# Kernel tuning notes

Hardware: AMD Instinct MI355X
Metric: run time of the kernel (lower is better)

## Reference

```python
import jax, jax.numpy as jnp
import numpy as np

B, T, D, H = 2, 2048, 1024, 16
HD = D // H            # 64
FH = 2752              # SwiGLU hidden: round64(int(2*4*D/3))
BETA_INIT = 0.5


def rmsnorm(x, w, eps=1e-6):
    x32 = x.astype(jnp.float32)
    r = jax.lax.rsqrt(jnp.mean(x32 * x32, axis=-1, keepdims=True) + eps)
    return (x32 * r).astype(x.dtype) * w


def rope(x, cos, sin):
    # x: (B,H,T,HD); cos/sin: (T,HD//2)
    d2 = x.shape[-1] // 2
    x1, x2 = x[..., :d2], x[..., d2:]
    return jnp.concatenate([x1 * cos - x2 * sin, x2 * cos + x1 * sin], axis=-1)


def delta_res(x, h, gn_w, g_w, g_b, wv_w, eps_k=1e-6):
    # k-hat = normalize(h); k = k_hat / sqrt(d)
    h32 = h.astype(jnp.float32)
    nrm = jnp.sqrt(jnp.sum(h32 * h32, axis=-1, keepdims=True))
    k = (h32 / jnp.maximum(nrm, eps_k)).astype(x.dtype) * (1.0 / np.sqrt(D))
    c = rmsnorm(x, gn_w)
    logit = c @ g_w + g_b                                   # (B,T)
    beta = (2.0 * jax.nn.sigmoid(logit.astype(jnp.float32))).astype(x.dtype)[..., None]
    v = jax.nn.sigmoid(x @ wv_w)[..., None]                 # (B,T,1)
    kTx = jnp.sum(k * x, axis=-1, keepdims=True)
    return x + beta * (v - kTx) * k


def setup_inputs() -> dict:
    key = jax.random.key(0)
    ks = jax.random.split(key, 12)
    s = 0.02
    gb = np.float32(np.log(BETA_INIT / 2.0 / (1.0 - BETA_INIT / 2.0 + 1e-8)))
    return {
        "x": jax.random.normal(ks[0], (B, T, D), jnp.float32),
        "wq": jax.random.normal(ks[1], (D, D), jnp.float32) * s,
        "wk": jax.random.normal(ks[2], (D, D), jnp.float32) * s,
        "wv": jax.random.normal(ks[3], (D, D), jnp.float32) * s,
        "wo": jax.random.normal(ks[4], (D, D), jnp.float32) * s,
        "qn_w": jnp.ones((HD,), jnp.float32),
        "kn_w": jnp.ones((HD,), jnp.float32),
        "attn_norm_w": jnp.ones((D,), jnp.float32),
        "g1_norm_w": jnp.ones((D,), jnp.float32),
        "g1_w": jax.random.normal(ks[5], (D,), jnp.float32) * s,
        "g1_b": jnp.asarray(gb),
        "wv1": jax.random.normal(ks[6], (D,), jnp.float32) * s,
        "mlp_norm_w": jnp.ones((D,), jnp.float32),
        "w1": jax.random.normal(ks[7], (FH, D), jnp.float32) * s,
        "w2": jax.random.normal(ks[8], (D, FH), jnp.float32) * s,
        "w3": jax.random.normal(ks[9], (FH, D), jnp.float32) * s,
        "g2_norm_w": jnp.ones((D,), jnp.float32),
        "g2_w": jax.random.normal(ks[10], (D,), jnp.float32) * s,
        "g2_b": jnp.asarray(gb),
        "wv2": jax.random.normal(ks[11], (D,), jnp.float32) * s,
    }


def reference(x, wq, wk, wv, wo, qn_w, kn_w, attn_norm_w,
              g1_norm_w, g1_w, g1_b, wv1, mlp_norm_w, w1, w2, w3,
              g2_norm_w, g2_w, g2_b, wv2):
    # ---- attention sublayer (pre-norm) ----
    xc = rmsnorm(x, attn_norm_w)
    q = (xc @ wq.T).reshape(B, T, H, HD).swapaxes(1, 2)   # (B,H,T,HD)
    k = (xc @ wk.T).reshape(B, T, H, HD).swapaxes(1, 2)
    v = (xc @ wv.T).reshape(B, T, H, HD).swapaxes(1, 2)
    q = rmsnorm(q, qn_w)
    k = rmsnorm(k, kn_w)
    inv_freq = 1.0 / (10000.0 ** (jnp.arange(0, HD, 2, dtype=jnp.float32) / HD))
    freqs = jnp.arange(T, dtype=jnp.float32)[:, None] * inv_freq[None, :]  # (T,HD/2)
    cos, sin = jnp.cos(freqs), jnp.sin(freqs)
    q = rope(q, cos, sin)
    k = rope(k, cos, sin)
    scale = 1.0 / np.sqrt(HD)
    scores = jnp.einsum('bhqd,bhkd->bhqk', q, k) * scale
    causal = jnp.where(jnp.arange(T)[:, None] >= jnp.arange(T)[None, :], 0.0, -jnp.inf).astype(scores.dtype)
    attn = jax.nn.softmax(scores + causal, axis=-1)
    out = jnp.einsum('bhqk,bhkd->bhqd', attn, v)
    h_attn = out.swapaxes(1, 2).reshape(B, T, D) @ wo.T
    x = delta_res(x, h_attn, g1_norm_w, g1_w, g1_b, wv1)
    # ---- MLP sublayer (pre-norm SwiGLU) ----
    xm = rmsnorm(x, mlp_norm_w)
    h_mlp = (jax.nn.silu(xm @ w1.T) * (xm @ w3.T)) @ w2.T
    x = delta_res(x, h_mlp, g2_norm_w, g2_w, g2_b, wv2)
    return x
```

## Files before the change

kernel.cpp:

```cpp
#include <hip/hip_runtime.h>
#include <hip/hip_bf16.h>
#include <math.h>

using bf16 = __hip_bfloat16;
typedef __bf16 bf16x8 __attribute__((ext_vector_type(8)));
typedef float f32x4 __attribute__((ext_vector_type(4)));

static constexpr int B_ = 2, T_ = 2048, D_ = 1024, H_ = 16, HD_ = 64, FH_ = 2752;
static constexpr int BT = B_ * T_;

struct __align__(8)  bh4 { bf16 h[4]; };
struct __align__(16) bh8 { bf16 h[8]; };

#define DEV static __device__ __forceinline__

DEV float b2f(bf16 v) { return __bfloat162float(v); }
DEV bf16  f2b(float v) { return __float2bfloat16(v); }
DEV __bf16 f2bb(float f) { __hip_bfloat16 h = __float2bfloat16(f); return *reinterpret_cast<__bf16*>(&h); }
DEV float sigmoidf_(float x) { return 1.0f / (1.0f + __expf(-x)); }

DEV void load4f(const bf16* p, float* v) {
    bh4 t = *reinterpret_cast<const bh4*>(p);
#pragma unroll
    for (int i = 0; i < 4; ++i) v[i] = b2f(t.h[i]);
}
DEV void load4f(const float* p, float* v) {
    float4 t = *reinterpret_cast<const float4*>(p);
    v[0] = t.x; v[1] = t.y; v[2] = t.z; v[3] = t.w;
}
DEV void store4(float* p, const float* v) {
    float4 t; t.x = v[0]; t.y = v[1]; t.z = v[2]; t.w = v[3];
    *reinterpret_cast<float4*>(p) = t;
}
DEV float waveReduceSum(float v) {
#pragma unroll
    for (int m = 32; m; m >>= 1) v += __shfl_xor(v, m);
    return v;
}

DEV void gl_lds16(const bf16* g, bf16* lds_base) {
    __builtin_amdgcn_global_load_lds(
        (const __attribute__((address_space(1))) void*)g,
        (__attribute__((address_space(3))) void*)lds_base, 16, 0, 0);
}

__global__ __launch_bounds__(256) void k_rope_tables(float* __restrict__ cost, float* __restrict__ sint) {
    int idx = blockIdx.x * 256 + threadIdx.x;
    if (idx >= T_ * 32) return;
    int t = idx >> 5, j = idx & 31;
    float inv = powf(10000.0f, -(float)j * (1.0f / 32.0f));
    float f = (float)t * inv;
    cost[idx] = cosf(f);
    sint[idx] = sinf(f);
}

__global__ __launch_bounds__(256) void k_f2b(const float* __restrict__ in, bf16* __restrict__ out, int n8) {
    int i = blockIdx.x * 256 + threadIdx.x;
    if (i >= n8) return;
    const float4* p = reinterpret_cast<const float4*>(in + (size_t)i * 8);
    float4 a = p[0], b = p[1];
    bh8 o;
    o.h[0] = f2b(a.x); o.h[1] = f2b(a.y); o.h[2] = f2b(a.z); o.h[3] = f2b(a.w);
    o.h[4] = f2b(b.x); o.h[5] = f2b(b.y); o.h[6] = f2b(b.z); o.h[7] = f2b(b.w);
    *reinterpret_cast<bh8*>(out + (size_t)i * 8) = o;
}

__global__ __launch_bounds__(256) void k_f2b_pair(const float* __restrict__ w1, const float* __restrict__ w3,
                                                  bf16* __restrict__ outp, int n8tot) {
    int i = blockIdx.x * 256 + threadIdx.x;
    if (i >= n8tot) return;
    int r = i >> 7, c8 = i & 127;
    int sel = (r >> 4) & 1;
    int j = ((r >> 5) << 4) | (r & 15);
    const float* src = (sel ? w3 : w1) + (size_t)j * D_ + c8 * 8;
    float4 a = reinterpret_cast<const float4*>(src)[0];
    float4 b = reinterpret_cast<const float4*>(src)[1];
    bh8 o;
    o.h[0] = f2b(a.x); o.h[1] = f2b(a.y); o.h[2] = f2b(a.z); o.h[3] = f2b(a.w);
    o.h[4] = f2b(b.x); o.h[5] = f2b(b.y); o.h[6] = f2b(b.z); o.h[7] = f2b(b.w);
    *reinterpret_cast<bh8*>(outp + (size_t)r * D_ + c8 * 8) = o;
}

__global__ __launch_bounds__(256) void k_rmsnorm(const float* __restrict__ x, const float* __restrict__ w,
                                                 bf16* __restrict__ out) {
    int row = blockIdx.x, tid = threadIdx.x;
    const float* xr = x + (size_t)row * D_;
    int base = tid * 4;
    float v[4];
    load4f(xr + base, v);
    float ss = v[0]*v[0] + v[1]*v[1] + v[2]*v[2] + v[3]*v[3];
    ss = waveReduceSum(ss);
    __shared__ float red[4];
    if ((tid & 63) == 0) red[tid >> 6] = ss;
    __syncthreads();
    ss = red[0] + red[1] + red[2] + red[3];
    float r = rsqrtf(ss * (1.0f / D_) + 1e-6f);
    float wv[4];
    load4f(w + base, wv);
    bh4 o;
#pragma unroll
    for (int i = 0; i < 4; ++i) o.h[i] = f2b(v[i] * r * wv[i]);
    *reinterpret_cast<bh4*>(out + (size_t)row * D_ + base) = o;
}

template <int BN, int EPI>
__global__ __launch_bounds__(256) void k_gemm_db(const bf16* __restrict__ A, const bf16* __restrict__ W,
                                                 bf16* __restrict__ C, int M, int N, int K) {
    constexpr int MR = (BN == 128) ? 4 : 2;
    constexpr int WR = (BN == 128) ? 64 : 32;
    __shared__ bf16 sA[2][128 * 32];
    __shared__ bf16 sB[2][BN * 32];
    int tid = threadIdx.x, lane = tid & 63, wid = tid >> 6;
    int m0 = blockIdx.x * 128, n0 = blockIdx.y * BN;
    int wr, wc;
    if (BN == 128) { wr = wid >> 1; wc = wid & 1; } else { wr = wid; wc = 0; }
    int l16 = lane & 15, lg = lane >> 4;
    int srow = lane >> 2;
    int scol = ((lane & 3) ^ (srow & 3)) * 8;
    int rchunk = (lg ^ (l16 & 3)) * 8;

    f32x4 acc[MR][4] = {};

#define STAGE(buf, k0)                                                                  \
    {                                                                                   \
        _Pragma("unroll")                                                               \
        for (int c = 0; c < 2; ++c) {                                                   \
            int r0 = wid * 32 + c * 16;                                                 \
            gl_lds16(&A[(size_t)(m0 + r0 + srow) * K + (k0) + scol], &sA[buf][r0 * 32]);\
        }                                                                               \
        if (BN == 128) {                                                                \
            _Pragma("unroll")                                                           \
            for (int c = 0; c < 2; ++c) {                                               \
                int r0 = wid * 32 + c * 16;                                             \
                int nrow = n0 + r0 + srow;                                              \
                if (nrow > N - 1) nrow = N - 1;                                         \
                gl_lds16(&W[(size_t)nrow * K + (k0) + scol], &sB[buf][r0 * 32]);        \
            }                                                                           \
        } else {                                                                        \
            int r0 = wid * 16;                                                          \
            int nrow = n0 + r0 + srow;                                                  \
            if (nrow > N - 1) nrow = N - 1;                                             \
            gl_lds16(&W[(size_t)nrow * K + (k0) + scol], &sB[buf][r0 * 32]);            \
        }                                                                               \
    }

    STAGE(0, 0);
    __syncthreads();
    int nk = K >> 5;
    int cur = 0;
    for (int t = 0; t < nk; ++t) {
        if (t + 1 < nk) STAGE(cur ^ 1, (t + 1) * 32);
        bf16x8 af[MR], bfr[4];
#pragma unroll
        for (int m = 0; m < MR; ++m)
            af[m] = *reinterpret_cast<const bf16x8*>(&sA[cur][(wr * WR + m * 16 + l16) * 32 + rchunk]);
#pragma unroll
        for (int n = 0; n < 4; ++n)
            bfr[n] = *reinterpret_cast<const bf16x8*>(&sB[cur][(wc * 64 + n * 16 + l16) * 32 + rchunk]);
#pragma unroll
        for (int m = 0; m < MR; ++m)
#pragma unroll
            for (int n = 0; n < 4; ++n)
                acc[m][n] = __builtin_amdgcn_mfma_f32_16x16x32_bf16(af[m], bfr[n], acc[m][n], 0, 0, 0);
        __syncthreads();
        cur ^= 1;
    }
#undef STAGE

    int rbase = m0 + wr * WR, cbase = n0 + wc * 64;
    if (EPI == 1) {
        int Ng = N >> 1;
        int gbase = (n0 >> 1) + wc * 32;
#pragma unroll
        for (int m = 0; m < MR; ++m) {
#pragma unroll
            for (int n2 = 0; n2 < 2; ++n2) {
                int gcol = gbase + n2 * 16 + l16;
#pragma unroll
                for (int r = 0; r < 4; ++r) {
                    int row = rbase + m * 16 + lg * 4 + r;
                    float a1 = acc[m][n2 * 2][r];
                    float a3 = acc[m][n2 * 2 + 1][r];
                    C[(size_t)row * Ng + gcol] = f2b(a1 * sigmoidf_(a1) * a3);
                }
            }
        }
    } else {
#pragma unroll
        for (int m = 0; m < MR; ++m) {
#pragma unroll
            for (int n = 0; n < 4; ++n) {
                int col = cbase + n * 16 + l16;
                if (col < N) {
#pragma unroll
                    for (int r = 0; r < 4; ++r) {
                        int row = rbase + m * 16 + lg * 4 + r;
                        C[(size_t)row * N + col] = f2b(acc[m][n][r]);
                    }
                }
            }
        }
    }
}

__global__ __launch_bounds__(256) void k_qk_norm_rope(const bf16* __restrict__ qin, const float* __restrict__ wn,
                                                      const float* __restrict__ cost, const float* __restrict__ sint,
                                                      bf16* __restrict__ qout, float scale, int ld, int off) {
    int tid = threadIdx.x;
    int g = blockIdx.x * 4 + (tid >> 6);
    int d = tid & 63;
    int h = g % H_, t = (g / H_) % T_, b = g / (H_ * T_);
    float v = b2f(qin[(size_t)(b * T_ + t) * ld + off + h * HD_ + d]);
    float ss = waveReduceSum(v * v);
    float r = rsqrtf(ss * (1.0f / HD_) + 1e-6f);
    float xn = v * r * wn[d];
    float p = __shfl_xor(xn, 32);
    float c = cost[t * 32 + (d & 31)], s = sint[t * 32 + (d & 31)];
    float o = (d < 32) ? (xn * c - p * s) : (xn * c + p * s);
    qout[((size_t)(b * H_ + h) * T_ + t) * HD_ + d] = f2b(o * scale);
}

__global__ __launch_bounds__(256) void k_v_transpose(const bf16* __restrict__ vin, bf16* __restrict__ vt,
                                                     int ld, int off) {
    __shared__ bf16 tile[64][72];
    int tid = threadIdx.x;
    int bh = blockIdx.y;
    int t0 = blockIdx.x * 64;
    int b = bh >> 4, h = bh & 15;
#pragma unroll
    for (int i = 0; i < 16; ++i) {
        int lin = i * 256 + tid;
        int tl = lin >> 6, d = lin & 63;
        tile[tl][d] = vin[(size_t)(b * T_ + t0 + tl) * ld + off + h * HD_ + d];
    }
    __syncthreads();
#pragma unroll
    for (int i = 0; i < 16; ++i) {
        int lin = i * 256 + tid;
        int d = lin >> 6, tl = lin & 63;
        vt[((size_t)bh * HD_ + d) * T_ + t0 + tl] = tile[tl][d];
    }
}

template <bool MASKED>
DEV void fa3_tile(const bf16* __restrict__ kl, const bf16* __restrict__ vl,
                  int l16, int lg, int qloc,
                  const bf16x8 qf0, const bf16x8 qf1,
                  f32x4* acc, float& m_r, float& l_r) {
    f32x4 s[8];
#pragma unroll
    for (int n = 0; n < 8; ++n) {
        int kv = n * 16 + l16;
        bf16x8 kf0 = *reinterpret_cast<const bf16x8*>(&kl[kv * 64 + (((lg ^ kv) & 7) << 3)]);
        bf16x8 kf1 = *reinterpret_cast<const bf16x8*>(&kl[kv * 64 + ((((4 + lg) ^ kv) & 7) << 3)]);
        f32x4 t = {};
        t = __builtin_amdgcn_mfma_f32_16x16x32_bf16(kf0, qf0, t, 0, 0, 0);
        t = __builtin_amdgcn_mfma_f32_16x16x32_bf16(kf1, qf1, t, 0, 0, 0);
        s[n] = t;
    }
    if (MASKED) {
#pragma unroll
        for (int n = 0; n < 8; ++n)
#pragma unroll
            for (int r = 0; r < 4; ++r)
                if (n * 16 + lg * 4 + r > qloc) s[n][r] = -INFINITY;
    }
    float mx = -INFINITY;
#pragma unroll
    for (int n = 0; n < 8; ++n)
#pragma unroll
        for (int r = 0; r < 4; ++r) mx = fmaxf(mx, s[n][r]);
    mx = fmaxf(mx, __shfl_xor(mx, 16));
    mx = fmaxf(mx, __shfl_xor(mx, 32));
    float mnew = fmaxf(m_r, mx);
    float corr = __expf(m_r - mnew);
    m_r = mnew;
    float ps = 0.0f;
#pragma unroll
    for (int n = 0; n < 8; ++n)
#pragma unroll
        for (int r = 0; r < 4; ++r) {
            float e = __expf(s[n][r] - mnew);
            s[n][r] = e;
            ps += e;
        }
    l_r = l_r * corr + ps;
#pragma unroll
    for (int np = 0; np < 4; ++np) acc[np] = acc[np] * corr;

    bf16x8 pb[4];
#pragma unroll
    for (int n2 = 0; n2 < 4; ++n2)
#pragma unroll
        for (int j = 0; j < 8; ++j)
            pb[n2][j] = f2bb(s[2 * n2 + (j >> 2)][j & 3]);

    int d15 = l16;
    int eoff = (lg & 1) * 4;
#pragma unroll
    for (int n2 = 0; n2 < 4; ++n2) {
        int c0 = (n2 * 4 + (lg >> 1));
        int c1 = c0 + 2;
#pragma unroll
        for (int np = 0; np < 4; ++np) {
            int d = np * 16 + l16;
            union { bf16x8 v; bh4 q[2]; } u;
            u.q[0] = *reinterpret_cast<const bh4*>(&vl[d * 128 + ((c0 ^ d15) << 3) + eoff]);
            u.q[1] = *reinterpret_cast<const bh4*>(&vl[d * 128 + ((c1 ^ d15) << 3) + eoff]);
            acc[np] = __builtin_amdgcn_mfma_f32_16x16x32_bf16(u.v, pb[n2], acc[np], 0, 0, 0);
        }
    }
}

__global__ __launch_bounds__(256) void k_flash(const bf16* __restrict__ Q, const bf16* __restrict__ Kk,
                                               const bf16* __restrict__ Vt, bf16* __restrict__ Out) {
    __shared__ bf16 kl[128 * 64];
    __shared__ bf16 vl[64 * 128];
    int tid = threadIdx.x, lane = tid & 63, w = tid >> 6;
    int l16 = lane & 15, lg = lane >> 4;
    int L = blockIdx.x;
    int xcd = L & 7, m = L >> 3;
    int bh = xcd * 4 + (m & 3);
    int qi = (T_ / 128 - 1) - (m >> 2);
    int q0 = qi * 128;
    int b = bh >> 4, h = bh & 15;
    const bf16* qb = Q + (size_t)bh * T_ * HD_;
    const bf16* kb = Kk + (size_t)bh * T_ * HD_;
    const bf16* vb = Vt + (size_t)bh * HD_ * T_;

    bf16x8 qfr[2][2];
#pragma unroll
    for (int f = 0; f < 2; ++f) {
        int qrow = q0 + w * 32 + f * 16 + l16;
        const bf16* qp = qb + (size_t)qrow * HD_ + lg * 8;
        qfr[f][0] = *reinterpret_cast<const bf16x8*>(qp);
        qfr[f][1] = *reinterpret_cast<const bf16x8*>(qp + 32);
    }
    f32x4 acc[2][4] = {};
    float m_r[2] = {-INFINITY, -INFINITY};
    float l_r[2] = {0.0f, 0.0f};

    for (int kv0 = 0; kv0 <= q0; kv0 += 128) {
        __syncthreads();
#pragma unroll
        for (int i = 0; i < 4; ++i) {
            int idx = i * 256 + tid;
            int kv = idx >> 3, c = idx & 7;
            *reinterpret_cast<bh8*>(&kl[kv * 64 + (((c ^ kv) & 7) << 3)]) =
                *reinterpret_cast<const bh8*>(&kb[(size_t)(kv0 + kv) * HD_ + c * 8]);
        }
#pragma unroll
        for (int i = 0; i < 4; ++i) {
            int idx = i * 256 + tid;
            int d = idx >> 4, c = idx & 15;
            *reinterpret_cast<bh8*>(&vl[d * 128 + (((c ^ d) & 15) << 3)]) =
                *reinterpret_cast<const bh8*>(&vb[(size_t)d * T_ + kv0 + c * 8]);
        }
        __syncthreads();
        if (kv0 == q0) {
#pragma unroll
            for (int f = 0; f < 2; ++f)
                fa3_tile<true>(kl, vl, l16, lg, w * 32 + f * 16 + l16,
                               qfr[f][0], qfr[f][1], acc[f], m_r[f], l_r[f]);
        } else {
#pragma unroll
            for (int f = 0; f < 2; ++f)
                fa3_tile<false>(kl, vl, l16, lg, 0,
                                qfr[f][0], qfr[f][1], acc[f], m_r[f], l_r[f]);
        }
    }
#pragma unroll
    for (int f = 0; f < 2; ++f) {
        float lt = l_r[f];
        lt += __shfl_xor(lt, 16);
        lt += __shfl_xor(lt, 32);
        float inv = 1.0f / lt;
        int qrow = q0 + w * 32 + f * 16 + l16;
#pragma unroll
        for (int np = 0; np < 4; ++np) {
            bh4 o;
#pragma unroll
            for (int r = 0; r < 4; ++r) o.h[r] = f2b(acc[f][np][r] * inv);
            *reinterpret_cast<bh4*>(&Out[(size_t)(b * T_ + qrow) * D_ + h * HD_ + np * 16 + lg * 4]) = o;
        }
    }
}

template <typename TIN, typename TOUT>
__global__ __launch_bounds__(256) void k_delta_res(const TIN* __restrict__ x, const bf16* __restrict__ h,
                                                   const float* __restrict__ gn_w, const float* __restrict__ g_w,
                                                   const float* __restrict__ g_b, const float* __restrict__ wv_w,
                                                   TOUT* __restrict__ out) {
    int row = blockIdx.x, tid = threadIdx.x;
    int base = tid * 4;
    float xv[4], hv[4], gnv[4], gwv[4], wvv[4];
    load4f(x + (size_t)row * D_ + base, xv);
    load4f(h + (size_t)row * D_ + base, hv);
    load4f(gn_w + base, gnv);
    load4f(g_w + base, gwv);
    load4f(wv_w + base, wvv);
    float s_h2 = 0, s_x2 = 0, s_xg = 0, s_xv = 0, s_hx = 0;
#pragma unroll
    for (int i = 0; i < 4; ++i) {
        s_h2 += hv[i] * hv[i];
        s_x2 += xv[i] * xv[i];
        s_xg += xv[i] * gnv[i] * gwv[i];
        s_xv += xv[i] * wvv[i];
        s_hx += hv[i] * xv[i];
    }
    s_h2 = waveReduceSum(s_h2); s_x2 = waveReduceSum(s_x2); s_xg = waveReduceSum(s_xg);
    s_xv = waveReduceSum(s_xv); s_hx = waveReduceSum(s_hx);
    __shared__ float red[4][5];
    int wid = tid >> 6;
    if ((tid & 63) == 0) {
        red[wid][0] = s_h2; red[wid][1] = s_x2; red[wid][2] = s_xg;
        red[wid][3] = s_xv; red[wid][4] = s_hx;
    }
    __syncthreads();
    s_h2 = red[0][0] + red[1][0] + red[2][0] + red[3][0];
    s_x2 = red[0][1] + red[1][1] + red[2][1] + red[3][1];
    s_xg = red[0][2] + red[1][2] + red[2][2] + red[3][2];
    s_xv = red[0][3] + red[1][3] + red[2][3] + red[3][3];
    s_hx = red[0][4] + red[1][4] + red[2][4] + red[3][4];

    float r = rsqrtf(s_x2 * (1.0f / D_) + 1e-6f);
    float logit = r * s_xg + g_b[0];
    float beta = 2.0f * sigmoidf_(logit);
    float vsig = sigmoidf_(s_xv);
    float nrm = sqrtf(s_h2);
    float ks = (1.0f / 32.0f) / fmaxf(nrm, 1e-6f);
    float coef = beta * (vsig - ks * s_hx) * ks;
    float o[4];
#pragma unroll
    for (int i = 0; i < 4; ++i) o[i] = xv[i] + coef * hv[i];
    store4(out + (size_t)row * D_ + base, o);
}

extern "C" void kernel_launch(void* const* d_in, const int* in_sizes, int n_in,
                              void* d_out, int out_size, void* d_ws, size_t ws_size,
                              hipStream_t stream) {
    const float* x       = (const float*)d_in[0];
    const float* wq      = (const float*)d_in[1];
    const float* wk      = (const float*)d_in[2];
    const float* wv      = (const float*)d_in[3];
    const float* wo      = (const float*)d_in[4];
    const float* qn_w    = (const float*)d_in[5];
    const float* kn_w    = (const float*)d_in[6];
    const float* attn_nw = (const float*)d_in[7];
    const float* g1_nw   = (const float*)d_in[8];
    const float* g1_w    = (const float*)d_in[9];
    const float* g1_b    = (const float*)d_in[10];
    const float* wv1     = (const float*)d_in[11];
    const float* mlp_nw  = (const float*)d_in[12];
    const float* w1      = (const float*)d_in[13];
    const float* w2      = (const float*)d_in[14];
    const float* w3      = (const float*)d_in[15];
    const float* g2_nw   = (const float*)d_in[16];
    const float* g2_w    = (const float*)d_in[17];
    const float* g2_b    = (const float*)d_in[18];
    const float* wv2     = (const float*)d_in[19];
    float* out = (float*)d_out;

    char* ws = (char*)d_ws;
    const size_t KB = 1024;
    const size_t MB = 1024 * 1024;
    float* cost = (float*)(ws);
    float* sint = (float*)(ws + 256 * KB);
    bf16* XC = (bf16*)(ws + 512 * KB);
    bf16* Bb = (bf16*)(ws + 512 * KB + 8  * MB);
    bf16* Cb = (bf16*)(ws + 512 * KB + 16 * MB);
    bf16* Db = (bf16*)(ws + 512 * KB + 24 * MB);
    bf16* Eb = (bf16*)(ws + 512 * KB + 32 * MB);
    bf16* Fb = (bf16*)(ws + 512 * KB + 40 * MB);
    bf16* Gb = (bf16*)(ws + 512 * KB + 48 * MB);
    float* x1 = (float*)(ws + 512 * KB + 56 * MB);

    bf16* wqkv = Eb;
    bf16* qkv  = Bb;
    bf16* wbo  = XC;
    bf16* attn_out = Bb;
    bf16* wpair = Bb;
    bf16* w2b  = Db;
    bf16* g    = Eb;
    bf16* hmlp = XC;

    const int nDD = D_ * D_ / 8, nFD = FH_ * D_ / 8;
    dim3 blk(256);

    k_rope_tables<<<dim3((T_ * 32) / 256), blk, 0, stream>>>(cost, sint);

    k_rmsnorm<<<dim3(BT), blk, 0, stream>>>(x, attn_nw, XC);
    k_f2b<<<dim3((nDD + 255) / 256), blk, 0, stream>>>(wq, wqkv, nDD);
    k_f2b<<<dim3((nDD + 255) / 256), blk, 0, stream>>>(wk, wqkv + (size_t)D_ * D_, nDD);
    k_f2b<<<dim3((nDD + 255) / 256), blk, 0, stream>>>(wv, wqkv + (size_t)2 * D_ * D_, nDD);

    dim3 gqkv(BT / 128, 3 * D_ / 128);
    k_gemm_db<128, 0><<<gqkv, blk, 0, stream>>>(XC, wqkv, qkv, BT, 3 * D_, D_);

    k_qk_norm_rope<<<dim3(BT * H_ / 4), blk, 0, stream>>>(qkv, qn_w, cost, sint, Eb, 0.125f, 3 * D_, 0);
    k_qk_norm_rope<<<dim3(BT * H_ / 4), blk, 0, stream>>>(qkv, kn_w, cost, sint, Fb, 1.0f, 3 * D_, D_);
    k_v_transpose<<<dim3(T_ / 64, B_ * H_), blk, 0, stream>>>(qkv, Gb, 3 * D_, 2 * D_);

    k_f2b<<<dim3((nDD + 255) / 256), blk, 0, stream>>>(wo, wbo, nDD);
    k_flash<<<dim3((T_ / 128) * B_ * H_), blk, 0, stream>>>(Eb, Fb, Gb, attn_out);

    dim3 gwo(BT / 128, D_ / 64);
    k_gemm_db<64, 0><<<gwo, blk, 0, stream>>>(attn_out, wbo, Cb, BT, D_, D_);

    k_delta_res<float, float><<<dim3(BT), blk, 0, stream>>>(x, Cb, g1_nw, g1_w, g1_b, wv1, x1);

    k_f2b_pair<<<dim3((2 * nFD + 255) / 256), blk, 0, stream>>>(w1, w3, wpair, 2 * nFD);
    k_f2b<<<dim3((nFD + 255) / 256), blk, 0, stream>>>(w2, w2b, nFD);

    k_rmsnorm<<<dim3(BT), blk, 0, stream>>>(x1, mlp_nw, XC);

    dim3 gffn(BT / 128, (2 * FH_) / 128);
    k_gemm_db<128, 1><<<gffn, blk, 0, stream>>>(XC, wpair, g, BT, 2 * FH_, D_);

    dim3 gw2(BT / 128, D_ / 64);
    k_gemm_db<64, 0><<<gw2, blk, 0, stream>>>(g, w2b, hmlp, BT, D_, FH_);

    k_delta_res<float, float><<<dim3(BT), blk, 0, stream>>>(x1, hmlp, g2_nw, g2_w, g2_b, wv2, out);
}
```

Baseline: 284.7 us.

## Use 256x128 GEMM tiles with grid swizzle and fuse MLP rmsnorm into delta_res

The QKV and FFN-up GEMMs now use a 512-thread kernel with 256x128 tiles, and the two N=1024 GEMMs use a dedicated 128x64 kernel. Both kernels remap block indices through an XCD-aware grid swizzle, and the LDS swizzle pattern is changed. The separate MLP rmsnorm launch is folded into the first delta_res kernel, which now also writes the normalized bf16 activations. The goals are more reuse per tile, better L2 locality across chiplets, and one fewer kernel launch and pass over memory. The trade-offs are higher register and LDS pressure per block, and the N-bounds clamps are removed.

```diff
diff --git a/kernel.cpp b/kernel.cpp
--- a/kernel.cpp
+++ b/kernel.cpp
@@ -103,45 +103,35 @@
     *reinterpret_cast<bh4*>(out + (size_t)row * D_ + base) = o;
 }
 
-template <int BN, int EPI>
-__global__ __launch_bounds__(256) void k_gemm_db(const bf16* __restrict__ A, const bf16* __restrict__ W,
+template <int EPI>
+__global__ __launch_bounds__(512) void k_gemm256(const bf16* __restrict__ A, const bf16* __restrict__ W,
                                                  bf16* __restrict__ C, int M, int N, int K) {
-    constexpr int MR = (BN == 128) ? 4 : 2;
-    constexpr int WR = (BN == 128) ? 64 : 32;
-    __shared__ bf16 sA[2][128 * 32];
-    __shared__ bf16 sB[2][BN * 32];
+    __shared__ bf16 sA[2][256 * 32];
+    __shared__ bf16 sB[2][128 * 32];
     int tid = threadIdx.x, lane = tid & 63, wid = tid >> 6;
-    int m0 = blockIdx.x * 128, n0 = blockIdx.y * BN;
-    int wr, wc;
-    if (BN == 128) { wr = wid >> 1; wc = wid & 1; } else { wr = wid; wc = 0; }
+    int nwg = gridDim.x;
+    int swz = (blockIdx.x & 7) * (nwg >> 3) + (blockIdx.x >> 3);
+    int gxm = M >> 8;
+    int m0 = (swz % gxm) * 256, n0 = (swz / gxm) * 128;
+    int wr = wid >> 1, wc = wid & 1;
     int l16 = lane & 15, lg = lane >> 4;
     int srow = lane >> 2;
-    int scol = ((lane & 3) ^ (srow & 3)) * 8;
-    int rchunk = (lg ^ (l16 & 3)) * 8;
-
-    f32x4 acc[MR][4] = {};
-
-#define STAGE(buf, k0)                                                                  \
-    {                                                                                   \
-        _Pragma("unroll")                                                               \
-        for (int c = 0; c < 2; ++c) {                                                   \
-            int r0 = wid * 32 + c * 16;                                                 \
-            gl_lds16(&A[(size_t)(m0 + r0 + srow) * K + (k0) + scol], &sA[buf][r0 * 32]);\
-        }                                                                               \
-        if (BN == 128) {                                                                \
-            _Pragma("unroll")                                                           \
-            for (int c = 0; c < 2; ++c) {                                               \
-                int r0 = wid * 32 + c * 16;                                             \
-                int nrow = n0 + r0 + srow;                                              \
-                if (nrow > N - 1) nrow = N - 1;                                         \
-                gl_lds16(&W[(size_t)nrow * K + (k0) + scol], &sB[buf][r0 * 32]);        \
-            }                                                                           \
-        } else {                                                                        \
-            int r0 = wid * 16;                                                          \
-            int nrow = n0 + r0 + srow;                                                  \
-            if (nrow > N - 1) nrow = N - 1;                                             \
-            gl_lds16(&W[(size_t)nrow * K + (k0) + scol], &sB[buf][r0 * 32]);            \
-        }                                                                               \
+    int scol = ((lane & 3) ^ ((lane >> 3) & 3)) * 8;
+    int rchunk = (lg ^ ((l16 >> 1) & 3)) * 8;
+
+    f32x4 acc[4][4] = {};
+
+#define STAGE(buf, k0)                                                                   \
+    {                                                                                    \
+        _Pragma("unroll")                                                                \
+        for (int c = 0; c < 2; ++c) {                                                    \
+            int r0 = wid * 32 + c * 16;                                                  \
+            gl_lds16(&A[(size_t)(m0 + r0 + srow) * K + (k0) + scol], &sA[buf][r0 * 32]); \
+        }                                                                                \
+        {                                                                                \
+            int r0 = wid * 16;                                                           \
+            gl_lds16(&W[(size_t)(n0 + r0 + srow) * K + (k0) + scol], &sB[buf][r0 * 32]); \
+        }                                                                                \
     }
 
     STAGE(0, 0);
@@ -150,15 +140,15 @@
     int cur = 0;
     for (int t = 0; t < nk; ++t) {
         if (t + 1 < nk) STAGE(cur ^ 1, (t + 1) * 32);
-        bf16x8 af[MR], bfr[4];
-#pragma unroll
-        for (int m = 0; m < MR; ++m)
-            af[m] = *reinterpret_cast<const bf16x8*>(&sA[cur][(wr * WR + m * 16 + l16) * 32 + rchunk]);
+        bf16x8 af[4], bfr[4];
+#pragma unroll
+        for (int m = 0; m < 4; ++m)
+            af[m] = *reinterpret_cast<const bf16x8*>(&sA[cur][(wr * 64 + m * 16 + l16) * 32 + rchunk]);
 #pragma unroll
         for (int n = 0; n < 4; ++n)
             bfr[n] = *reinterpret_cast<const bf16x8*>(&sB[cur][(wc * 64 + n * 16 + l16) * 32 + rchunk]);
 #pragma unroll
-        for (int m = 0; m < MR; ++m)
+        for (int m = 0; m < 4; ++m)
 #pragma unroll
             for (int n = 0; n < 4; ++n)
                 acc[m][n] = __builtin_amdgcn_mfma_f32_16x16x32_bf16(af[m], bfr[n], acc[m][n], 0, 0, 0);
@@ -167,12 +157,12 @@
     }
 #undef STAGE
 
-    int rbase = m0 + wr * WR, cbase = n0 + wc * 64;
+    int rbase = m0 + wr * 64;
     if (EPI == 1) {
         int Ng = N >> 1;
         int gbase = (n0 >> 1) + wc * 32;
 #pragma unroll
-        for (int m = 0; m < MR; ++m) {
+        for (int m = 0; m < 4; ++m) {
 #pragma unroll
             for (int n2 = 0; n2 < 2; ++n2) {
                 int gcol = gbase + n2 * 16 + l16;
@@ -186,18 +176,85 @@
             }
         }
     } else {
-#pragma unroll
-        for (int m = 0; m < MR; ++m) {
+        int cbase = n0 + wc * 64;
+#pragma unroll
+        for (int m = 0; m < 4; ++m) {
 #pragma unroll
             for (int n = 0; n < 4; ++n) {
                 int col = cbase + n * 16 + l16;
-                if (col < N) {
-#pragma unroll
-                    for (int r = 0; r < 4; ++r) {
-                        int row = rbase + m * 16 + lg * 4 + r;
-                        C[(size_t)row * N + col] = f2b(acc[m][n][r]);
-                    }
+#pragma unroll
+                for (int r = 0; r < 4; ++r) {
+                    int row = rbase + m * 16 + lg * 4 + r;
+                    C[(size_t)row * N + col] = f2b(acc[m][n][r]);
                 }
+            }
+        }
+    }
+}
+
+__global__ __launch_bounds__(256) void k_gemm64(const bf16* __restrict__ A, const bf16* __restrict__ W,
+                                                bf16* __restrict__ C, int M, int N, int K) {
+    __shared__ bf16 sA[2][128 * 32];
+    __shared__ bf16 sB[2][64 * 32];
+    int tid = threadIdx.x, lane = tid & 63, wid = tid >> 6;
+    int nwg = gridDim.x;
+    int swz = (blockIdx.x & 7) * (nwg >> 3) + (blockIdx.x >> 3);
+    int gxm = M >> 7;
+    int m0 = (swz % gxm) * 128, n0 = (swz / gxm) * 64;
+    int wr = wid;
+    int l16 = lane & 15, lg = lane >> 4;
+    int srow = lane >> 2;
+    int scol = ((lane & 3) ^ ((lane >> 3) & 3)) * 8;
+    int rchunk = (lg ^ ((l16 >> 1) & 3)) * 8;
+
+    f32x4 acc[2][4] = {};
+
+#define STAGE(buf, k0)                                                                   \
+    {                                                                                    \
+        _Pragma("unroll")                                                                \
+        for (int c = 0; c < 2; ++c) {                                                    \
+            int r0 = wid * 32 + c * 16;                                                  \
+            gl_lds16(&A[(size_t)(m0 + r0 + srow) * K + (k0) + scol], &sA[buf][r0 * 32]); \
+        }                                                                                \
+        {                                                                                \
+            int r0 = wid * 16;                                                           \
+            gl_lds16(&W[(size_t)(n0 + r0 + srow) * K + (k0) + scol], &sB[buf][r0 * 32]); \
+        }                                                                                \
+    }
+
+    STAGE(0, 0);
+    __syncthreads();
+    int nk = K >> 5;
+    int cur = 0;
+    for (int t = 0; t < nk; ++t) {
+        if (t + 1 < nk) STAGE(cur ^ 1, (t + 1) * 32);
+        bf16x8 af[2], bfr[4];
+#pragma unroll
+        for (int m = 0; m < 2; ++m)
+            af[m] = *reinterpret_cast<const bf16x8*>(&sA[cur][(wr * 32 + m * 16 + l16) * 32 + rchunk]);
+#pragma unroll
+        for (int n = 0; n < 4; ++n)
+            bfr[n] = *reinterpret_cast<const bf16x8*>(&sB[cur][(n * 16 + l16) * 32 + rchunk]);
+#pragma unroll
+        for (int m = 0; m < 2; ++m)
+#pragma unroll
+            for (int n = 0; n < 4; ++n)
+                acc[m][n] = __builtin_amdgcn_mfma_f32_16x16x32_bf16(af[m], bfr[n], acc[m][n], 0, 0, 0);
+        __syncthreads();
+        cur ^= 1;
+    }
+#undef STAGE
+
+    int rbase = m0 + wr * 32;
+#pragma unroll
+    for (int m = 0; m < 2; ++m) {
+#pragma unroll
+        for (int n = 0; n < 4; ++n) {
+            int col = n0 + n * 16 + l16;
+#pragma unroll
+            for (int r = 0; r < 4; ++r) {
+                int row = rbase + m * 16 + lg * 4 + r;
+                C[(size_t)row * N + col] = f2b(acc[m][n][r]);
             }
         }
     }
@@ -386,11 +443,12 @@
     }
 }
 
-template <typename TIN, typename TOUT>
-__global__ __launch_bounds__(256) void k_delta_res(const TIN* __restrict__ x, const bf16* __restrict__ h,
+template <int WRITE_XM>
+__global__ __launch_bounds__(256) void k_delta_res(const float* __restrict__ x, const bf16* __restrict__ h,
                                                    const float* __restrict__ gn_w, const float* __restrict__ g_w,
                                                    const float* __restrict__ g_b, const float* __restrict__ wv_w,
-                                                   TOUT* __restrict__ out) {
+                                                   float* __restrict__ out,
+                                                   bf16* __restrict__ xm_out, const float* __restrict__ mlp_w) {
     int row = blockIdx.x, tid = threadIdx.x;
     int base = tid * 4;
     float xv[4], hv[4], gnv[4], gwv[4], wvv[4];
@@ -434,6 +492,23 @@
 #pragma unroll
     for (int i = 0; i < 4; ++i) o[i] = xv[i] + coef * hv[i];
     store4(out + (size_t)row * D_ + base, o);
+
+    if (WRITE_XM) {
+        float s2 = o[0]*o[0] + o[1]*o[1] + o[2]*o[2] + o[3]*o[3];
+        s2 = waveReduceSum(s2);
+        __shared__ float red2[4];
+        __syncthreads();
+        if ((tid & 63) == 0) red2[wid] = s2;
+        __syncthreads();
+        s2 = red2[0] + red2[1] + red2[2] + red2[3];
+        float rr = rsqrtf(s2 * (1.0f / D_) + 1e-6f);
+        float mw[4];
+        load4f(mlp_w + base, mw);
+        bh4 ob;
+#pragma unroll
+        for (int i = 0; i < 4; ++i) ob.h[i] = f2b(o[i] * rr * mw[i]);
+        *reinterpret_cast<bh4*>(xm_out + (size_t)row * D_ + base) = ob;
+    }
 }
 
 extern "C" void kernel_launch(void* const* d_in, const int* in_sizes, int n_in,
@@ -494,8 +569,7 @@
     k_f2b<<<dim3((nDD + 255) / 256), blk, 0, stream>>>(wk, wqkv + (size_t)D_ * D_, nDD);
     k_f2b<<<dim3((nDD + 255) / 256), blk, 0, stream>>>(wv, wqkv + (size_t)2 * D_ * D_, nDD);
 
-    dim3 gqkv(BT / 128, 3 * D_ / 128);
-    k_gemm_db<128, 0><<<gqkv, blk, 0, stream>>>(XC, wqkv, qkv, BT, 3 * D_, D_);
+    k_gemm256<0><<<dim3(16 * 24), dim3(512), 0, stream>>>(XC, wqkv, qkv, BT, 3 * D_, D_);
 
     k_qk_norm_rope<<<dim3(BT * H_ / 4), blk, 0, stream>>>(qkv, qn_w, cost, sint, Eb, 0.125f, 3 * D_, 0);
     k_qk_norm_rope<<<dim3(BT * H_ / 4), blk, 0, stream>>>(qkv, kn_w, cost, sint, Fb, 1.0f, 3 * D_, D_);
@@ -504,21 +578,16 @@
     k_f2b<<<dim3((nDD + 255) / 256), blk, 0, stream>>>(wo, wbo, nDD);
     k_flash<<<dim3((T_ / 128) * B_ * H_), blk, 0, stream>>>(Eb, Fb, Gb, attn_out);
 
-    dim3 gwo(BT / 128, D_ / 64);
-    k_gemm_db<64, 0><<<gwo, blk, 0, stream>>>(attn_out, wbo, Cb, BT, D_, D_);
-
-    k_delta_res<float, float><<<dim3(BT), blk, 0, stream>>>(x, Cb, g1_nw, g1_w, g1_b, wv1, x1);
+    k_gemm64<<<dim3(32 * 16), blk, 0, stream>>>(attn_out, wbo, Cb, BT, D_, D_);
+
+    k_delta_res<1><<<dim3(BT), blk, 0, stream>>>(x, Cb, g1_nw, g1_w, g1_b, wv1, x1, XC, mlp_nw);
 
     k_f2b_pair<<<dim3((2 * nFD + 255) / 256), blk, 0, stream>>>(w1, w3, wpair, 2 * nFD);
     k_f2b<<<dim3((nFD + 255) / 256), blk, 0, stream>>>(w2, w2b, nFD);
 
-    k_rmsnorm<<<dim3(BT), blk, 0, stream>>>(x1, mlp_nw, XC);
-
-    dim3 gffn(BT / 128, (2 * FH_) / 128);
-    k_gemm_db<128, 1><<<gffn, blk, 0, stream>>>(XC, wpair, g, BT, 2 * FH_, D_);
-
-    dim3 gw2(BT / 128, D_ / 64);
-    k_gemm_db<64, 0><<<gw2, blk, 0, stream>>>(g, w2b, hmlp, BT, D_, FH_);
-
-    k_delta_res<float, float><<<dim3(BT), blk, 0, stream>>>(x1, hmlp, g2_nw, g2_w, g2_b, wv2, out);
-}
+    k_gemm256<1><<<dim3(16 * 43), dim3(512), 0, stream>>>(XC, wpair, g, BT, 2 * FH_, D_);
+
+    k_gemm64<<<dim3(32 * 16), blk, 0, stream>>>(g, w2b, hmlp, BT, D_, FH_);
+
+    k_delta_res<0><<<dim3(BT), blk, 0, stream>>>(x1, hmlp, g2_nw, g2_w, g2_b, wv2, out, nullptr, nullptr);
+}
```

Measured after the change: 290.7 us. 2.1% more time.
